# Kernel tuning notes

Measured on AMD Instinct MI355X. Metric: run time of the kernel, lower is better.

Reference implementation:

```python
import jax, jax.numpy as jnp
import numpy as np

D_K = 64


def setup_inputs() -> dict:
    key = jax.random.key(0)
    ks = jax.random.split(key, 5)
    B, S, D, H, DK, DV = 4, 2048, 1024, 16, 64, 64
    # xavier_normal-ish scale for the per-head projections
    std_qk = (2.0 / (D + DK)) ** 0.5
    std_o = (2.0 / (H * DV + D)) ** 0.5
    return {
        "x": jax.random.normal(ks[0], (B, S, D), dtype=jnp.float32),
        "W_Q": jax.random.normal(ks[1], (H, D, DK), dtype=jnp.float32) * std_qk,
        "W_K": jax.random.normal(ks[2], (H, D, DK), dtype=jnp.float32) * std_qk,
        "W_V": jax.random.normal(ks[3], (H, D, DV), dtype=jnp.float32) * std_qk,
        "W_O": jax.random.normal(ks[4], (H * DV, D), dtype=jnp.float32) * std_o,
    }


def reference(x, W_Q, W_K, W_V, W_O):
    # x: [B,S,D]; W_Q/W_K: [H,D,dk]; W_V: [H,D,dv]; W_O: [H*dv, D]
    q = jnp.einsum("bsd,hdk->bhsk", x, W_Q)
    k = jnp.einsum("bsd,hdk->bhsk", x, W_K)
    v = jnp.einsum("bsd,hdv->bhsv", x, W_V)
    scale = 1.0 / jnp.sqrt(jnp.asarray(D_K, dtype=x.dtype))
    scores = jnp.einsum("bhsk,bhtk->bhst", q, k) * scale  # [B,H,S,S]
    attn = jax.nn.softmax(scores, axis=-1)
    out = jnp.einsum("bhst,bhtv->bhsv", attn, v)  # [B,H,S,dv]
    B, H, S, DV = out.shape
    # concat heads along feature dim: head i occupies [i*dv:(i+1)*dv]
    out = jnp.transpose(out, (0, 2, 1, 3)).reshape(B, S, H * DV)
    return out @ W_O  # [B,S,D]
```

## Files before the change

### kernel.cpp

```cpp
#include <hip/hip_runtime.h>
#include <hip/hip_bf16.h>
#include <cstdint>
#include <cstddef>


typedef __attribute__((ext_vector_type(8))) __bf16 bf16v8;
typedef __attribute__((ext_vector_type(4))) float f32x4;
typedef __attribute__((ext_vector_type(16))) float f32x16;
typedef __attribute__((ext_vector_type(8))) unsigned short u16x8;
typedef __attribute__((ext_vector_type(4))) unsigned u32x4;
typedef unsigned short ushort_t;

#define AS3(p) ((__attribute__((address_space(3))) void*)(p))
#define AS1C(p) ((const __attribute__((address_space(1))) void*)(p))

__device__ __forceinline__ ushort_t f2bf(float f) {
  unsigned u = __builtin_bit_cast(unsigned, f);
  unsigned r = u + 0x7FFFu + ((u >> 16) & 1u);
  return (ushort_t)(r >> 16);
}

__device__ __forceinline__ unsigned cvt_pk_bf16(float lo, float hi) {
  unsigned r;
  asm("v_cvt_pk_bf16_f32 %0, %1, %2" : "=v"(r) : "v"(lo), "v"(hi));
  return r;
}

__device__ __forceinline__ void plswap(unsigned& x, unsigned& y) {
  asm("v_permlane32_swap_b32 %0, %1" : "+v"(x), "+v"(y));
}

__device__ __forceinline__ float exp2_raw(float x) {
  float r;
  asm("v_exp_f32 %0, %1" : "=v"(r) : "v"(x));
  return r;
}

constexpr int B_ = 4, S_ = 2048, D_ = 1024, H_ = 16, DK_ = 64;
constexpr int M_ = B_ * S_;
constexpr int NQKV_ = 3 * H_ * DK_;
constexpr float QSCALE = 0.125f * 1.44269504088896f;

__global__ __launch_bounds__(256) void cast_x_kernel(const float* __restrict__ x,
                                                     ushort_t* __restrict__ xb) {
  size_t i = (size_t)blockIdx.x * 256 + threadIdx.x;
  const float4* px = (const float4*)(x + i * 8);
  float4 a = px[0], b = px[1];
  u16x8 v;
  v[0] = f2bf(a.x); v[1] = f2bf(a.y); v[2] = f2bf(a.z); v[3] = f2bf(a.w);
  v[4] = f2bf(b.x); v[5] = f2bf(b.y); v[6] = f2bf(b.z); v[7] = f2bf(b.w);
  size_t di = i ^ ((i >> 8) & 3);
  *(u16x8*)(xb + di * 8) = v;
}

__global__ __launch_bounds__(256) void prep_wqkv_kernel(const float* __restrict__ Wq,
                                                        const float* __restrict__ Wk,
                                                        const float* __restrict__ Wv,
                                                        ushort_t* __restrict__ dst) {
  __shared__ ushort_t lt[64 * 264];
  const int t = threadIdx.x;
  const int blk = blockIdx.x;
  const int p = blk >> 6;
  const int rem = blk & 63;
  const int h = rem >> 2, d0 = (rem & 3) << 8;
  const float* W = (p == 0) ? Wq : ((p == 1) ? Wk : Wv);
  const float sc = (p == 0) ? QSCALE : 1.0f;
  const int rt = t >> 4, cq = (t & 15) << 2;
#pragma unroll
  for (int it = 0; it < 16; ++it) {
    int r = it * 16 + rt;
    float4 v = *(const float4*)(W + (h << 16) + (size_t)(d0 + r) * 64 + cq);
    lt[(cq + 0) * 264 + r] = f2bf(v.x * sc);
    lt[(cq + 1) * 264 + r] = f2bf(v.y * sc);
    lt[(cq + 2) * 264 + r] = f2bf(v.z * sc);
    lt[(cq + 3) * 264 + r] = f2bf(v.w * sc);
  }
  __syncthreads();
  const int c8 = t & 31;
#pragma unroll
  for (int it = 0; it < 8; ++it) {
    int dk = it * 8 + (t >> 5);
    u16x8 v = *(const u16x8*)&lt[dk * 264 + c8 * 8];
    int s = (dk >> 1) & 3;
    *(u16x8*)(dst + ((p << 20) | (h << 16) | (dk << 10)) + d0 + ((c8 ^ s) << 3)) = v;
  }
}

__global__ __launch_bounds__(256) void prep_wo_kernel(const float* __restrict__ Wo,
                                                      ushort_t* __restrict__ dst) {
  __shared__ ushort_t lt[64 * 264];
  const int t = threadIdx.x;
  const int n0 = (blockIdx.x >> 2) << 6;
  const int k0 = (blockIdx.x & 3) << 8;
  const int rt = t >> 4, nq = (t & 15) << 2;
#pragma unroll
  for (int it = 0; it < 16; ++it) {
    int kr = it * 16 + rt;
    float4 v = *(const float4*)(Wo + (size_t)(k0 + kr) * 1024 + n0 + nq);
    lt[(nq + 0) * 264 + kr] = f2bf(v.x);
    lt[(nq + 1) * 264 + kr] = f2bf(v.y);
    lt[(nq + 2) * 264 + kr] = f2bf(v.z);
    lt[(nq + 3) * 264 + kr] = f2bf(v.w);
  }
  __syncthreads();
  const int c8 = t & 31;
#pragma unroll
  for (int it = 0; it < 8; ++it) {
    int nr = it * 8 + (t >> 5);
    u16x8 v = *(const u16x8*)&lt[nr * 264 + c8 * 8];
    int n = n0 + nr;
    int s = (n >> 1) & 3;
    *(u16x8*)(dst + (size_t)n * 1024 + k0 + ((c8 ^ s) << 3)) = v;
  }
}

#define VMW(N) asm volatile("s_waitcnt vmcnt(" N ")" ::: "memory")
#define BAR() asm volatile("s_barrier" ::: "memory")

#define STAGE3(T)                                                                   \
  {                                                                                 \
    const int pb = (((T) + 3) & 3) * 32768;                                         \
    __builtin_amdgcn_global_load_lds(AS1C(gA0), AS3(lds + pb + wid * 1024), 16, 0, 0); \
    __builtin_amdgcn_global_load_lds(AS1C(gA1), AS3(lds + pb + 8192 + wid * 1024), 16, 0, 0); \
    __builtin_amdgcn_global_load_lds(AS1C(gB0), AS3(lds + pb + 16384 + wid * 1024), 16, 0, 0); \
    __builtin_amdgcn_global_load_lds(AS1C(gB1), AS3(lds + pb + 24576 + wid * 1024), 16, 0, 0); \
    gA0 += 32; gA1 += 32; gB0 += 32; gB1 += 32;                                     \
  }

#define TILE_BODY(T, VMSTR, DO_STAGE)                                               \
  {                                                                                 \
    const int cb = ((T) & 3) * 32768;                                               \
    VMW(VMSTR);                                                                     \
    BAR();                                                                          \
    if (DO_STAGE) STAGE3(T);                                                        \
    bf16v8 af[8], bfr[4];                                                           \
    _Pragma("unroll")                                                               \
    for (int i = 0; i < 8; ++i)                                                     \
      af[i] = *(const bf16v8*)(lds + cb + awo + i * 1024);                          \
    _Pragma("unroll")                                                               \
    for (int j = 0; j < 4; ++j)                                                     \
      bfr[j] = *(const bf16v8*)(lds + cb + bwo + j * 1024);                         \
    __builtin_amdgcn_s_setprio(1);                                                  \
    _Pragma("unroll")                                                               \
    for (int i = 0; i < 8; ++i)                                                     \
      _Pragma("unroll")                                                             \
      for (int j = 0; j < 4; ++j)                                                   \
        acc[i][j] = __builtin_amdgcn_mfma_f32_16x16x32_bf16(af[i], bfr[j], acc[i][j], 0, 0, 0); \
    __builtin_amdgcn_s_setprio(0);                                                  \
  }

__global__ __launch_bounds__(512) void gemm256_qkv(
    const ushort_t* __restrict__ A, const ushort_t* __restrict__ Bt,
    ushort_t* __restrict__ qb, ushort_t* __restrict__ kb, ushort_t* __restrict__ vt) {
  extern __shared__ __align__(16) char lds[];
  const int tid = threadIdx.x;
  const int wid = tid >> 6, lane = tid & 63;
  const int g = lane >> 4, lq = lane & 15;
  const int wm = wid >> 2, wn = wid & 3;
  const int bid = blockIdx.x;
  const int wg = (bid & 7) * 48 + (bid >> 3);
  const int mb = wg / 12, nb = wg % 12;
  const int m0 = mb * 256, n0 = nb * 256;

  const int co = (g ^ ((lq >> 1) & 3)) * 16;
  const int awo = wm * 8192 + lq * 64 + co;
  const int bwo = 16384 + wn * 4096 + lq * 64 + co;

  const ushort_t* gA0 = A + (size_t)(m0 + (tid >> 2)) * 1024 + (tid & 3) * 8;
  const ushort_t* gA1 = gA0 + (size_t)128 * 1024;
  const ushort_t* gB0 = Bt + (size_t)(n0 + (tid >> 2)) * 1024 + (tid & 3) * 8;
  const ushort_t* gB1 = gB0 + (size_t)128 * 1024;

  f32x4 acc[8][4] = {};

  STAGE3(-3); STAGE3(-2); STAGE3(-1);

  for (int t = 0; t < 28; ++t) TILE_BODY(t, "8", true);
  TILE_BODY(28, "8", true);
  TILE_BODY(29, "8", false);
  TILE_BODY(30, "4", false);
  TILE_BODY(31, "0", false);

  asm volatile("s_waitcnt lgkmcnt(0)" ::: "memory");
  BAR();
  const int p = n0 >> 10;
  if (p == 2) {
#pragma unroll
    for (int i = 0; i < 8; ++i)
#pragma unroll
      for (int j = 0; j < 4; ++j) {
        int col = wn * 64 + j * 16 + lq;
        int swz = (col & 7) << 4;
#pragma unroll
        for (int r = 0; r < 4; ++r) {
          int row = wm * 128 + i * 16 + g * 4 + r;
          *(ushort_t*)(lds + ((col * 512 + row * 2) ^ swz)) = f2bf(acc[i][j][r]);
        }
      }
  } else {
#pragma unroll
    for (int i = 0; i < 8; ++i)
#pragma unroll
      for (int j = 0; j < 4; ++j) {
        int col = wn * 64 + j * 16 + lq;
#pragma unroll
        for (int r = 0; r < 4; ++r) {
          int row = wm * 128 + i * 16 + g * 4 + r;
          *(ushort_t*)(lds + ((row * 512 + col * 2) ^ ((row & 7) << 4))) = f2bf(acc[i][j][r]);
        }
      }
  }
  asm volatile("s_waitcnt lgkmcnt(0)" ::: "memory");
  BAR();

  if (p == 0) {
#pragma unroll
    for (int it = 0; it < 16; ++it) {
      int ci = it * 512 + tid;
      int row = ci >> 5, ch = ci & 31;
      u16x8 v = *(const u16x8*)(lds + ((row * 512 + ch * 16) ^ ((row & 7) << 4)));
      int gcol = n0 + ch * 8;
      int h = (gcol >> 6) & 15, dd0 = gcol & 63;
      int grow = m0 + row;
      int b = grow >> 11, s = grow & 2047;
      size_t bh = (size_t)(b * 16 + h);
      *(u16x8*)(qb + (bh * 2048 + s) * 64 + dd0) = v;
    }
  } else if (p == 1) {
#pragma unroll
    for (int it = 0; it < 16; ++it) {
      int ci = it * 512 + tid;
      int row = ci >> 5, ch = ci & 31;
      u16x8 v = *(const u16x8*)(lds + ((row * 512 + ch * 16) ^ ((row & 7) << 4)));
      int gcol = n0 + ch * 8;
      int h = (gcol >> 6) & 15, dd0 = gcol & 63;
      int grow = m0 + row;
      int b = grow >> 11, s = grow & 2047;
      size_t bh = (size_t)(b * 16 + h);
      int tt = s >> 6, sIn = s & 63;
      int byte = (sIn * 128 + dd0 * 2) ^ ((sIn & 15) << 4);
      *(u16x8*)((char*)kb + (((size_t)bh * 32 + tt) << 13) + byte) = v;
    }
  } else {
#pragma unroll
    for (int it = 0; it < 16; ++it) {
      int ci = it * 512 + tid;
      int crow = ci >> 5, ch = ci & 31;
      u16x8 v = *(const u16x8*)(lds + ((crow * 512 + ch * 16) ^ ((crow & 7) << 4)));
      int gcol = n0 + crow;
      int h = (gcol >> 6) & 15, dd = gcol & 63;
      int grow = m0 + ch * 8;
      int b = grow >> 11, s = grow & 2047;
      size_t bh = (size_t)(b * 16 + h);
      int tt = s >> 6, sIn0 = s & 63;
      int byte = (dd * 128 + sIn0 * 2) ^ ((dd & 15) << 4);
      *(u16x8*)((char*)vt + (((size_t)bh * 32 + tt) << 13) + byte) = v;
    }
  }
}

#define PSTAGE(T)                                                                   \
  {                                                                                 \
    const int pb = ((T) & 3) * 16384;                                               \
    __builtin_amdgcn_global_load_lds(AS1C(gA0), AS3(lds + pb + wid * 1024), 16, 0, 0); \
    __builtin_amdgcn_global_load_lds(AS1C(gA1), AS3(lds + pb + 4096 + wid * 1024), 16, 0, 0); \
    __builtin_amdgcn_global_load_lds(AS1C(gB0), AS3(lds + pb + 8192 + wid * 1024), 16, 0, 0); \
    __builtin_amdgcn_global_load_lds(AS1C(gB1), AS3(lds + pb + 12288 + wid * 1024), 16, 0, 0); \
    gA0 += 32; gA1 += 32; gB0 += 32; gB1 += 32;                                     \
  }

#define PBODY(T, VMSTR, DO_STAGE)                                                   \
  {                                                                                 \
    const int cb = ((T) & 3) * 16384;                                               \
    VMW(VMSTR);                                                                     \
    BAR();                                                                          \
    if (DO_STAGE) PSTAGE((T) + 3);                                                  \
    bf16v8 af[4], bfr[4];                                                           \
    _Pragma("unroll")                                                               \
    for (int i = 0; i < 4; ++i)                                                     \
      af[i] = *(const bf16v8*)(lds + cb + awo + i * 1024);                          \
    _Pragma("unroll")                                                               \
    for (int j = 0; j < 4; ++j)                                                     \
      bfr[j] = *(const bf16v8*)(lds + cb + bwo + j * 1024);                         \
    __builtin_amdgcn_s_setprio(1);                                                  \
    _Pragma("unroll")                                                               \
    for (int i = 0; i < 4; ++i)                                                     \
      _Pragma("unroll")                                                             \
      for (int j = 0; j < 4; ++j)                                                   \
        acc[i][j] = __builtin_amdgcn_mfma_f32_16x16x32_bf16(af[i], bfr[j], acc[i][j], 0, 0, 0); \
    __builtin_amdgcn_s_setprio(0);                                                  \
  }

__global__ __launch_bounds__(256) void gemm128_op(
    const ushort_t* __restrict__ A, const ushort_t* __restrict__ Bt,
    float* __restrict__ Cf) {
  extern __shared__ __align__(16) char lds[];
  const int tid = threadIdx.x;
  const int wid = tid >> 6, lane = tid & 63;
  const int g = lane >> 4, lq = lane & 15;
  const int wm = wid >> 1, wn = wid & 1;
  const int bid = blockIdx.x;
  const int wg = (bid & 7) * 64 + (bid >> 3);
  const int mb = wg >> 3, nb = wg & 7;
  const int m0 = mb * 128, n0 = nb * 128;

  const int co = (g ^ ((lq >> 1) & 3)) * 16;
  const int awo = wm * 4096 + lq * 64 + co;
  const int bwo = 8192 + wn * 4096 + lq * 64 + co;

  const ushort_t* gA0 = A + (size_t)(m0 + (tid >> 2)) * 1024 + (tid & 3) * 8;
  const ushort_t* gA1 = gA0 + (size_t)64 * 1024;
  const ushort_t* gB0 = Bt + (size_t)(n0 + (tid >> 2)) * 1024 + (tid & 3) * 8;
  const ushort_t* gB1 = gB0 + (size_t)64 * 1024;

  f32x4 acc[4][4] = {};

  PSTAGE(0); PSTAGE(1); PSTAGE(2);

  for (int t = 0; t < 29; ++t) PBODY(t, "8", true);
  PBODY(29, "8", false);
  PBODY(30, "4", false);
  PBODY(31, "0", false);

#pragma unroll
  for (int i = 0; i < 4; ++i)
#pragma unroll
    for (int j = 0; j < 4; ++j)
#pragma unroll
      for (int r = 0; r < 4; ++r) {
        int row = m0 + wm * 64 + i * 16 + g * 4 + r;
        int col = n0 + wn * 64 + j * 16 + lq;
        Cf[(size_t)row * 1024 + col] = acc[i][j][r];
      }
}

__device__ __forceinline__ void softpack(const f32x16& s0, const f32x16& s1,
                                         float& lsum, bf16v8& pa0, bf16v8& pa1,
                                         bf16v8& pa2, bf16v8& pa3) {
  float e0[16], e1[16];
#pragma unroll
  for (int r = 0; r < 16; ++r) e0[r] = exp2_raw(s0[r]);
#pragma unroll
  for (int r = 0; r < 16; ++r) e1[r] = exp2_raw(s1[r]);
  float ad[16];
#pragma unroll
  for (int r = 0; r < 16; ++r) ad[r] = e0[r] + e1[r];
#pragma unroll
  for (int st = 8; st >= 1; st >>= 1)
#pragma unroll
    for (int r = 0; r < st; ++r) ad[r] += ad[r + st];
  lsum += ad[0];
  unsigned a0 = cvt_pk_bf16(e0[0], e0[1]), b0 = cvt_pk_bf16(e0[4], e0[5]);
  unsigned a1 = cvt_pk_bf16(e0[2], e0[3]), b1 = cvt_pk_bf16(e0[6], e0[7]);
  unsigned a2 = cvt_pk_bf16(e0[8], e0[9]), b2 = cvt_pk_bf16(e0[12], e0[13]);
  unsigned a3 = cvt_pk_bf16(e0[10], e0[11]), b3 = cvt_pk_bf16(e0[14], e0[15]);
  unsigned a4 = cvt_pk_bf16(e1[0], e1[1]), b4 = cvt_pk_bf16(e1[4], e1[5]);
  unsigned a5 = cvt_pk_bf16(e1[2], e1[3]), b5 = cvt_pk_bf16(e1[6], e1[7]);
  unsigned a6 = cvt_pk_bf16(e1[8], e1[9]), b6 = cvt_pk_bf16(e1[12], e1[13]);
  unsigned a7 = cvt_pk_bf16(e1[10], e1[11]), b7 = cvt_pk_bf16(e1[14], e1[15]);
  plswap(a0, b0); plswap(a1, b1); plswap(a2, b2); plswap(a3, b3);
  plswap(a4, b4); plswap(a5, b5); plswap(a6, b6); plswap(a7, b7);
  pa0 = __builtin_bit_cast(bf16v8, u32x4{a0, a1, b0, b1});
  pa1 = __builtin_bit_cast(bf16v8, u32x4{a2, a3, b2, b3});
  pa2 = __builtin_bit_cast(bf16v8, u32x4{a4, a5, b4, b5});
  pa3 = __builtin_bit_cast(bf16v8, u32x4{a6, a7, b6, b7});
}

#define MFMA32(a, b, c) __builtin_amdgcn_mfma_f32_32x32x16_bf16(a, b, c, 0, 0, 0)

#define ASTAGE(T)                                                                   \
  {                                                                                 \
    const int pb = ((T) & 1) * 16384;                                               \
    const char* ks = kbase + ((size_t)(T) << 13);                                   \
    const char* vs = vbase + ((size_t)(T) << 13);                                   \
    _Pragma("unroll")                                                               \
    for (int j = 0; j < 2; ++j) {                                                   \
      __builtin_amdgcn_global_load_lds(AS1C(ks + w * 2048 + j * 1024 + lane * 16),  \
                                       AS3(smem + pb + w * 2048 + j * 1024), 16, 0, 0); \
      __builtin_amdgcn_global_load_lds(AS1C(vs + w * 2048 + j * 1024 + lane * 16),  \
                                       AS3(smem + pb + 8192 + w * 2048 + j * 1024), 16, 0, 0); \
    }                                                                               \
  }

#define ACOMPUTE(T)                                                                 \
  {                                                                                 \
    const char* bk = smem + ((T) & 1) * 16384;                                      \
    bf16v8 kf0[4], kf1[4], vfr[2][4];                                               \
    _Pragma("unroll")                                                               \
    for (int c = 0; c < 4; ++c) {                                                   \
      kf0[c] = *(const bf16v8*)(bk + addr4[c]);                                     \
      kf1[c] = *(const bf16v8*)(bk + addr4[c] + 4096);                              \
    }                                                                               \
    _Pragma("unroll")                                                               \
    for (int nb = 0; nb < 2; ++nb)                                                  \
      _Pragma("unroll")                                                             \
      for (int ks2 = 0; ks2 < 4; ++ks2)                                             \
        vfr[nb][ks2] = *(const bf16v8*)(bk + addr4[ks2] + 8192 + nb * 4096);        \
    f32x16 s0 = {}, s1 = {};                                                        \
    __builtin_amdgcn_s_setprio(1);                                                  \
    _Pragma("unroll")                                                               \
    for (int c = 0; c < 4; ++c) {                                                   \
      s0 = MFMA32(kf0[c], qf[c], s0);                                               \
      s1 = MFMA32(kf1[c], qf[c], s1);                                               \
    }                                                                               \
    __builtin_amdgcn_s_setprio(0);                                                  \
    bf16v8 pa0, pa1, pa2, pa3;                                                      \
    softpack(s0, s1, lsum, pa0, pa1, pa2, pa3);                                     \
    __builtin_amdgcn_s_setprio(1);                                                  \
    _Pragma("unroll")                                                               \
    for (int nb = 0; nb < 2; ++nb) {                                                \
      oa[nb] = MFMA32(pa0, vfr[nb][0], oa[nb]);                                     \
      oa[nb] = MFMA32(pa1, vfr[nb][1], oa[nb]);                                     \
      oa[nb] = MFMA32(pa2, vfr[nb][2], oa[nb]);                                     \
      oa[nb] = MFMA32(pa3, vfr[nb][3], oa[nb]);                                     \
    }                                                                               \
    __builtin_amdgcn_s_setprio(0);                                                  \
  }

__global__ __launch_bounds__(256) void attn_kernel(const ushort_t* __restrict__ qb,
                                                   const ushort_t* __restrict__ kt,
                                                   const ushort_t* __restrict__ vt,
                                                   ushort_t* __restrict__ aout) {
  __shared__ __align__(16) char smem[32768];
  __shared__ float cbuf[4][32];
  const int tid = threadIdx.x;
  const int w = tid >> 6, lane = tid & 63;
  const int hi = lane >> 5, l31 = lane & 31;
  const int bidx = blockIdx.x;
  const int xcd = bidx & 7, slot = bidx >> 3;
  const int bh = xcd + 8 * (slot >> 4);
  const int qt = (slot & 15) * 4 + w;
  const char* kbase = (const char*)kt + ((size_t)bh << 18);
  const char* vbase = (const char*)vt + ((size_t)bh << 18);
  const ushort_t* Qp = qb + (size_t)bh * (S_ * 64) + qt * 32 * 64;

  bf16v8 qf[4];
#pragma unroll
  for (int c = 0; c < 4; ++c)
    qf[c] = *(const bf16v8*)(Qp + l31 * 64 + c * 16 + hi * 8);

  int addr4[4];
#pragma unroll
  for (int c = 0; c < 4; ++c)
    addr4[c] = (l31 * 128 + c * 32 + hi * 16) ^ ((l31 & 15) << 4);

  f32x16 oa[2] = {};
  float lsum = 0.f;

  ASTAGE(0);

#pragma unroll 2
  for (int t = 0; t < 31; ++t) {
    BAR();
    ASTAGE(t + 1);
    VMW("4");
    BAR();
    ACOMPUTE(t);
  }
  BAR();
  VMW("0");
  BAR();
  ACOMPUTE(31);

  lsum += __shfl_xor(lsum, 32);
  ushort_t* ob = (ushort_t*)(smem + w * 4096);
  cbuf[w][l31] = 1.0f / lsum;
  asm volatile("s_waitcnt lgkmcnt(0)" ::: "memory");
#pragma unroll
  for (int rq = 0; rq < 4; ++rq) {
    f32x4 c4 = *(const f32x4*)&cbuf[w][8 * rq + 4 * hi];
#pragma unroll
    for (int j = 0; j < 4; ++j) {
      int row = 8 * rq + 4 * hi + j;
#pragma unroll
      for (int nb = 0; nb < 2; ++nb)
        ob[row * 64 + nb * 32 + l31] = f2bf(oa[nb][4 * rq + j] * c4[j]);
    }
  }
  asm volatile("s_waitcnt lgkmcnt(0)" ::: "memory");
  const int row = lane >> 1, hf = lane & 1;
  const int b = bh >> 4, h = bh & 15;
  const int rowg = b * 2048 + qt * 32 + row;
  const int sx = (rowg >> 1) & 3;
  size_t rbase = (size_t)rowg * 1024;
#pragma unroll
  for (int i = 0; i < 4; ++i) {
    bf16v8 v = *(const bf16v8*)&ob[row * 64 + hf * 32 + i * 8];
    int c = h * 8 + hf * 4 + i;
    *(bf16v8*)(aout + rbase + (size_t)((c ^ sx) * 8)) = v;
  }
}

extern "C" void kernel_launch(void* const* d_in, const int* in_sizes, int n_in,
                              void* d_out, int out_size, void* d_ws, size_t ws_size,
                              hipStream_t stream) {
  const float* x = (const float*)d_in[0];
  const float* Wq = (const float*)d_in[1];
  const float* Wk = (const float*)d_in[2];
  const float* Wv = (const float*)d_in[3];
  const float* Wo = (const float*)d_in[4];
  float* out = (float*)d_out;

  char* ws = (char*)d_ws;
  constexpr size_t OFF_XB = 0;
  constexpr size_t OFF_WQKV = 16777216;
  constexpr size_t OFF_WO = 23068672;
  constexpr size_t OFF_Q = 25165824;
  constexpr size_t OFF_K = 41943040;
  constexpr size_t OFF_V = 58720256;
  constexpr size_t OFF_AO = 75497472;
  constexpr size_t WS_NEEDED = 92274688;
  if (ws_size < WS_NEEDED) return;

  ushort_t* xb = (ushort_t*)(ws + OFF_XB);
  ushort_t* wqkv_t = (ushort_t*)(ws + OFF_WQKV);
  ushort_t* wo_t = (ushort_t*)(ws + OFF_WO);
  ushort_t* q_buf = (ushort_t*)(ws + OFF_Q);
  ushort_t* k_t = (ushort_t*)(ws + OFF_K);
  ushort_t* v_t = (ushort_t*)(ws + OFF_V);
  ushort_t* a_out = (ushort_t*)(ws + OFF_AO);

  cast_x_kernel<<<(M_ * D_ / 8) / 256, 256, 0, stream>>>(x, xb);
  prep_wqkv_kernel<<<192, 256, 0, stream>>>(Wq, Wk, Wv, wqkv_t);
  prep_wo_kernel<<<64, 256, 0, stream>>>(Wo, wo_t);

  gemm256_qkv<<<(M_ / 256) * (NQKV_ / 256), 512, 131072, stream>>>(
      xb, wqkv_t, q_buf, k_t, v_t);

  attn_kernel<<<1024, 256, 0, stream>>>(q_buf, k_t, v_t, a_out);

  gemm128_op<<<(M_ / 128) * (D_ / 128), 256, 65536, stream>>>(a_out, wo_t, out);
}
```

Measured before the change: 195.0 us.

## Shrink QKV GEMM LDS to double buffering and split epilogue into halves

The QKV GEMM drops from a 4-stage to a 2-stage LDS ring (128KB to 64KB dynamic shared memory), with a barrier before each stage and the load overlapped with the previous tile's compute. The epilogue now writes the output tile through LDS in two 128-row phases so it fits in the smaller buffer. The goal is to let two workgroups fit per CU and raise occupancy, at the cost of shallower prefetch, an extra barrier per k-step and more epilogue barriers.

```diff
diff --git a/kernel.cpp b/kernel.cpp
--- a/kernel.cpp
+++ b/kernel.cpp
@@ -116,10 +116,11 @@
 
 #define VMW(N) asm volatile("s_waitcnt vmcnt(" N ")" ::: "memory")
 #define BAR() asm volatile("s_barrier" ::: "memory")
-
-#define STAGE3(T)                                                                   \
+#define LGKM0() asm volatile("s_waitcnt lgkmcnt(0)" ::: "memory")
+
+#define QSTAGE(T)                                                                   \
   {                                                                                 \
-    const int pb = (((T) + 3) & 3) * 32768;                                         \
+    const int pb = ((T) & 1) * 32768;                                               \
     __builtin_amdgcn_global_load_lds(AS1C(gA0), AS3(lds + pb + wid * 1024), 16, 0, 0); \
     __builtin_amdgcn_global_load_lds(AS1C(gA1), AS3(lds + pb + 8192 + wid * 1024), 16, 0, 0); \
     __builtin_amdgcn_global_load_lds(AS1C(gB0), AS3(lds + pb + 16384 + wid * 1024), 16, 0, 0); \
@@ -127,12 +128,9 @@
     gA0 += 32; gA1 += 32; gB0 += 32; gB1 += 32;                                     \
   }
 
-#define TILE_BODY(T, VMSTR, DO_STAGE)                                               \
+#define QCOMP(T)                                                                    \
   {                                                                                 \
-    const int cb = ((T) & 3) * 32768;                                               \
-    VMW(VMSTR);                                                                     \
-    BAR();                                                                          \
-    if (DO_STAGE) STAGE3(T);                                                        \
+    const int cb = ((T) & 1) * 32768;                                               \
     bf16v8 af[8], bfr[4];                                                           \
     _Pragma("unroll")                                                               \
     for (int i = 0; i < 8; ++i)                                                     \
@@ -173,88 +171,97 @@
 
   f32x4 acc[8][4] = {};
 
-  STAGE3(-3); STAGE3(-2); STAGE3(-1);
-
-  for (int t = 0; t < 28; ++t) TILE_BODY(t, "8", true);
-  TILE_BODY(28, "8", true);
-  TILE_BODY(29, "8", false);
-  TILE_BODY(30, "4", false);
-  TILE_BODY(31, "0", false);
-
-  asm volatile("s_waitcnt lgkmcnt(0)" ::: "memory");
+  QSTAGE(0);
+
+  for (int t = 0; t < 31; ++t) {
+    BAR();
+    QSTAGE(t + 1);
+    VMW("4");
+    BAR();
+    QCOMP(t);
+  }
   BAR();
+  VMW("0");
+  BAR();
+  QCOMP(31);
+
   const int p = n0 >> 10;
-  if (p == 2) {
-#pragma unroll
-    for (int i = 0; i < 8; ++i)
-#pragma unroll
-      for (int j = 0; j < 4; ++j) {
-        int col = wn * 64 + j * 16 + lq;
-        int swz = (col & 7) << 4;
-#pragma unroll
-        for (int r = 0; r < 4; ++r) {
-          int row = wm * 128 + i * 16 + g * 4 + r;
-          *(ushort_t*)(lds + ((col * 512 + row * 2) ^ swz)) = f2bf(acc[i][j][r]);
-        }
+#pragma unroll
+  for (int ph = 0; ph < 2; ++ph) {
+    BAR();
+    if (wm == ph) {
+      if (p == 2) {
+#pragma unroll
+        for (int i = 0; i < 8; ++i)
+#pragma unroll
+          for (int j = 0; j < 4; ++j) {
+            int col = wn * 64 + j * 16 + lq;
+            int swz = (col & 7) << 4;
+#pragma unroll
+            for (int r = 0; r < 4; ++r) {
+              int rowrel = i * 16 + g * 4 + r;
+              *(ushort_t*)(lds + ((col * 256 + rowrel * 2) ^ swz)) = f2bf(acc[i][j][r]);
+            }
+          }
+      } else {
+#pragma unroll
+        for (int i = 0; i < 8; ++i)
+#pragma unroll
+          for (int j = 0; j < 4; ++j) {
+            int col = wn * 64 + j * 16 + lq;
+#pragma unroll
+            for (int r = 0; r < 4; ++r) {
+              int rowrel = i * 16 + g * 4 + r;
+              *(ushort_t*)(lds + ((rowrel * 512 + col * 2) ^ ((rowrel & 7) << 4))) = f2bf(acc[i][j][r]);
+            }
+          }
       }
-  } else {
-#pragma unroll
-    for (int i = 0; i < 8; ++i)
-#pragma unroll
-      for (int j = 0; j < 4; ++j) {
-        int col = wn * 64 + j * 16 + lq;
-#pragma unroll
-        for (int r = 0; r < 4; ++r) {
-          int row = wm * 128 + i * 16 + g * 4 + r;
-          *(ushort_t*)(lds + ((row * 512 + col * 2) ^ ((row & 7) << 4))) = f2bf(acc[i][j][r]);
-        }
+    }
+    LGKM0();
+    BAR();
+    if (p == 0) {
+#pragma unroll
+      for (int it = 0; it < 8; ++it) {
+        int ci = it * 512 + tid;
+        int rowrel = ci >> 5, ch = ci & 31;
+        u16x8 v = *(const u16x8*)(lds + ((rowrel * 512 + ch * 16) ^ ((rowrel & 7) << 4)));
+        int gcol = n0 + ch * 8;
+        int h = (gcol >> 6) & 15, dd0 = gcol & 63;
+        int grow = m0 + ph * 128 + rowrel;
+        int b = grow >> 11, s = grow & 2047;
+        size_t bh = (size_t)(b * 16 + h);
+        *(u16x8*)(qb + (bh * 2048 + s) * 64 + dd0) = v;
       }
-  }
-  asm volatile("s_waitcnt lgkmcnt(0)" ::: "memory");
-  BAR();
-
-  if (p == 0) {
-#pragma unroll
-    for (int it = 0; it < 16; ++it) {
-      int ci = it * 512 + tid;
-      int row = ci >> 5, ch = ci & 31;
-      u16x8 v = *(const u16x8*)(lds + ((row * 512 + ch * 16) ^ ((row & 7) << 4)));
-      int gcol = n0 + ch * 8;
-      int h = (gcol >> 6) & 15, dd0 = gcol & 63;
-      int grow = m0 + row;
-      int b = grow >> 11, s = grow & 2047;
-      size_t bh = (size_t)(b * 16 + h);
-      *(u16x8*)(qb + (bh * 2048 + s) * 64 + dd0) = v;
-    }
-  } else if (p == 1) {
-#pragma unroll
-    for (int it = 0; it < 16; ++it) {
-      int ci = it * 512 + tid;
-      int row = ci >> 5, ch = ci & 31;
-      u16x8 v = *(const u16x8*)(lds + ((row * 512 + ch * 16) ^ ((row & 7) << 4)));
-      int gcol = n0 + ch * 8;
-      int h = (gcol >> 6) & 15, dd0 = gcol & 63;
-      int grow = m0 + row;
-      int b = grow >> 11, s = grow & 2047;
-      size_t bh = (size_t)(b * 16 + h);
-      int tt = s >> 6, sIn = s & 63;
-      int byte = (sIn * 128 + dd0 * 2) ^ ((sIn & 15) << 4);
-      *(u16x8*)((char*)kb + (((size_t)bh * 32 + tt) << 13) + byte) = v;
-    }
-  } else {
-#pragma unroll
-    for (int it = 0; it < 16; ++it) {
-      int ci = it * 512 + tid;
-      int crow = ci >> 5, ch = ci & 31;
-      u16x8 v = *(const u16x8*)(lds + ((crow * 512 + ch * 16) ^ ((crow & 7) << 4)));
-      int gcol = n0 + crow;
-      int h = (gcol >> 6) & 15, dd = gcol & 63;
-      int grow = m0 + ch * 8;
-      int b = grow >> 11, s = grow & 2047;
-      size_t bh = (size_t)(b * 16 + h);
-      int tt = s >> 6, sIn0 = s & 63;
-      int byte = (dd * 128 + sIn0 * 2) ^ ((dd & 15) << 4);
-      *(u16x8*)((char*)vt + (((size_t)bh * 32 + tt) << 13) + byte) = v;
+    } else if (p == 1) {
+#pragma unroll
+      for (int it = 0; it < 8; ++it) {
+        int ci = it * 512 + tid;
+        int rowrel = ci >> 5, ch = ci & 31;
+        u16x8 v = *(const u16x8*)(lds + ((rowrel * 512 + ch * 16) ^ ((rowrel & 7) << 4)));
+        int gcol = n0 + ch * 8;
+        int h = (gcol >> 6) & 15, dd0 = gcol & 63;
+        int grow = m0 + ph * 128 + rowrel;
+        int b = grow >> 11, s = grow & 2047;
+        size_t bh = (size_t)(b * 16 + h);
+        int tt = s >> 6, sIn = s & 63;
+        int byte = (sIn * 128 + dd0 * 2) ^ ((sIn & 15) << 4);
+        *(u16x8*)((char*)kb + (((size_t)bh * 32 + tt) << 13) + byte) = v;
+      }
+    } else {
+#pragma unroll
+      for (int it = 0; it < 8; ++it) {
+        int ci = it * 512 + tid;
+        int crow = ci >> 4, chh = ci & 15;
+        u16x8 v = *(const u16x8*)(lds + ((crow * 256 + chh * 16) ^ ((crow & 7) << 4)));
+        int gcol = n0 + crow;
+        int h = (gcol >> 6) & 15, dd = gcol & 63;
+        int grow = m0 + ph * 128 + chh * 8;
+        int b = grow >> 11, s = grow & 2047;
+        size_t bh = (size_t)(b * 16 + h);
+        int tt = s >> 6, sIn0 = s & 63;
+        int byte = (dd * 128 + sIn0 * 2) ^ ((dd & 15) << 4);
+        *(u16x8*)((char*)vt + (((size_t)bh * 32 + tt) << 13) + byte) = v;
+      }
     }
   }
 }
@@ -524,7 +531,7 @@
   prep_wqkv_kernel<<<192, 256, 0, stream>>>(Wq, Wk, Wv, wqkv_t);
   prep_wo_kernel<<<64, 256, 0, stream>>>(Wo, wo_t);
 
-  gemm256_qkv<<<(M_ / 256) * (NQKV_ / 256), 512, 131072, stream>>>(
+  gemm256_qkv<<<(M_ / 256) * (NQKV_ / 256), 512, 65536, stream>>>(
       xb, wqkv_t, q_buf, k_t, v_t);
 
   attn_kernel<<<1024, 256, 0, stream>>>(q_buf, k_t, v_t, a_out);
```

Measured after the change: 198.4 us. No clear change (+1.7%).
